# Optimization experiments

Measured on AMD Instinct MI355X. Metric: run time of the kernel, lower is better.

The kernel has to match this reference:

```python
import math
import jax, jax.numpy as jnp
import numpy as np

B, S, D, H, E = 4, 1024, 1024, 16, 8
HD = D // H


def gelu_new(x):
    # BERT/GPT tanh-approx GELU (NewGELUActivation)
    c = math.sqrt(2.0 / math.pi)
    return 0.5 * x * (1.0 + jnp.tanh(c * (x + 0.044715 * x ** 3)))


def setup_inputs() -> dict:
    key = jax.random.key(0)
    ks = jax.random.split(key, 12)
    s = 0.02
    return {
        "x": jax.random.normal(ks[0], (B, S, D), jnp.float32),
        "Wq": jax.random.normal(ks[1], (D, D), jnp.float32) * s,
        "bq": jnp.zeros((D,), jnp.float32),
        "Wk": jax.random.normal(ks[2], (D, D), jnp.float32) * s,
        "bk": jnp.zeros((D,), jnp.float32),
        "Wv": jax.random.normal(ks[3], (D, D), jnp.float32) * s,
        "bv": jnp.zeros((D,), jnp.float32),
        "Wg": jax.random.normal(ks[4], (D, E), jnp.float32) * s,
        "bg": jnp.zeros((E,), jnp.float32),
        "W1": jax.random.normal(ks[5], (E, D, D), jnp.float32) * s,
        "b1": jnp.zeros((E, D), jnp.float32),
        "W2": jax.random.normal(ks[6], (E, D, D), jnp.float32) * s,
        "b2": jnp.zeros((E, D), jnp.float32),
    }


def reference(x, Wq, bq, Wk, bk, Wv, bv, Wg, bg, W1, b1, W2, b2):
    b = x.shape[0]
    # ---- Attention (faithful to original: no head transpose, so attention
    # is computed ACROSS HEADS per token: scores are [B,S,H,H]) ----
    Q = (x @ Wq + bq).reshape(b, -1, H, HD)
    K = (x @ Wk + bk).reshape(b, -1, H, HD)
    V = (x @ Wv + bv).reshape(b, -1, H, HD)
    scores = jnp.einsum('bsqd,bskd->bsqk', Q, K) / (HD ** 0.5)  # [B,S,H,H]
    attn = jax.nn.softmax(scores, axis=-1)
    out = jnp.einsum('bsqk,bskd->bsqd', attn, V)  # [B,S,H,HD]
    # torch: out.transpose(1,2).contiguous().view(B,-1,H*HD)
    a = jnp.transpose(out, (0, 2, 1, 3)).reshape(b, -1, D)  # [B,S,D]

    # ---- ComplexMoE: dense all-experts + sequence-mean gating ----
    gates = jax.nn.softmax(a.mean(axis=1) @ Wg + bg, axis=-1)  # [B,E]
    h = gelu_new(jnp.einsum('bsd,edh->bseh', a, W1) + b1)       # [B,S,E,D]
    eo = jnp.einsum('bseh,ehf->bsef', h, W2) + b2               # [B,S,E,D]
    return jnp.einsum('be,bsed->bsd', gates, eo)                # [B,S,D]
```

## Files before the change

kernel.cpp:

```cpp
#include <hip/hip_runtime.h>
#include <stdint.h>

#define AS1 __attribute__((address_space(1)))
#define AS3 __attribute__((address_space(3)))

typedef short v8s __attribute__((ext_vector_type(8)));
typedef float v4f __attribute__((ext_vector_type(4)));

__device__ __forceinline__ float b2f(unsigned short u) {
  return __uint_as_float(((unsigned int)u) << 16);
}
__device__ __forceinline__ unsigned short f2bu(float f) {
  unsigned int u = __float_as_uint(f);
  u += 0x7fffu + ((u >> 16) & 1u);
  return (unsigned short)(u >> 16);
}

__device__ __forceinline__ void gload16(const void* g, const void* l) {
  __builtin_amdgcn_global_load_lds(
      (const AS1 void*)(uintptr_t)g,
      (AS3 void*)(unsigned)(uintptr_t)l,
      16, 0, 0);
}

#define BAR __builtin_amdgcn_s_barrier()
#define VMC2 asm volatile("s_waitcnt vmcnt(2)" ::: "memory")
#define VMC0 asm volatile("s_waitcnt vmcnt(0)" ::: "memory")

__global__ __launch_bounds__(256)
void transpose_cvt(const float* __restrict__ src, long long srcZ,
                   unsigned short* __restrict__ dst, long long dstZ, int ld_dst,
                   int K, int N)
{
  __shared__ float t[64][65];
  const int e = blockIdx.z;
  src += (long long)e * srcZ;
  dst += (long long)e * dstZ;
  const int k0 = blockIdx.y * 64, n0 = blockIdx.x * 64;
  const int tr  = threadIdx.x >> 4;
  const int tc4 = (threadIdx.x & 15) * 4;
#pragma unroll
  for (int p = 0; p < 4; ++p) {
    float4 v = *(const float4*)(src + (long long)(k0 + tr + p * 16) * N + n0 + tc4);
    t[tr + p * 16][tc4 + 0] = v.x;
    t[tr + p * 16][tc4 + 1] = v.y;
    t[tr + p * 16][tc4 + 2] = v.z;
    t[tr + p * 16][tc4 + 3] = v.w;
  }
  __syncthreads();
#pragma unroll
  for (int p = 0; p < 4; ++p) {
    const int n = tr + p * 16;
    ushort4 o;
    o.x = f2bu(t[tc4 + 0][n]);
    o.y = f2bu(t[tc4 + 1][n]);
    o.z = f2bu(t[tc4 + 2][n]);
    o.w = f2bu(t[tc4 + 3][n]);
    *(ushort4*)(dst + (long long)(n0 + n) * ld_dst + k0 + tc4) = o;
  }
}

__global__ __launch_bounds__(256)
void cvt_f32_bf16(const float* __restrict__ src, unsigned short* __restrict__ dst, int n)
{
  const int i = (blockIdx.x * 256 + threadIdx.x) * 4;
  if (i >= n) return;
  float4 v = *(const float4*)(src + i);
  ushort4 o;
  o.x = f2bu(v.x); o.y = f2bu(v.y); o.z = f2bu(v.z); o.w = f2bu(v.w);
  *(ushort4*)(dst + i) = o;
}

template<int MH>
__device__ __forceinline__ void read_a(v8s af[4][2],
    const unsigned short* pa, int wm, int rswz)
{
#pragma unroll
  for (int i = 0; i < 4; ++i)
#pragma unroll
    for (int s = 0; s < 2; ++s)
      af[i][s] = *(const v8s*)(pa + MH*8192 + ((((wm*4 + i)*2 + s) << 9) | rswz));
}

template<int NH>
__device__ __forceinline__ void read_b(v8s bfr[2][2],
    const unsigned short* pb, int wn, int rswz)
{
#pragma unroll
  for (int j = 0; j < 2; ++j)
#pragma unroll
    for (int s = 0; s < 2; ++s)
      bfr[j][s] = *(const v8s*)(pb + NH*8192 + ((((wn*2 + j)*2 + s) << 9) | rswz));
}

template<int MH, int NH>
__device__ __forceinline__ void mfma16(v4f acc[8][4], v8s af[4][2], v8s bfr[2][2])
{
  __builtin_amdgcn_s_setprio(1);
#pragma unroll
  for (int i = 0; i < 4; ++i)
#pragma unroll
    for (int j = 0; j < 2; ++j)
#pragma unroll
      for (int s = 0; s < 2; ++s)
        acc[MH*4+i][NH*2+j] = __builtin_amdgcn_mfma_f32_16x16x32_bf16(
            af[i][s], bfr[j][s], acc[MH*4+i][NH*2+j], 0, 0, 0);
  __builtin_amdgcn_s_setprio(0);
}

#define STAGE(G, LD, LDSBASE, GROW0, KT) do { \
    gload16((G) + (long long)((GROW0) + sRow) * (LD) + (KT) + sCol, \
            (LDSBASE) + w512); \
    gload16((G) + (long long)((GROW0) + 64 + sRow) * (LD) + (KT) + sCol, \
            (LDSBASE) + 4096 + w512); \
  } while (0)

template<int EPI>
__global__ __launch_bounds__(512, 2)
void gemm256(const unsigned short* __restrict__ A, int lda,
             const unsigned short* __restrict__ Bt, int ldb,
             const float* __restrict__ bias,
             void* __restrict__ out0, unsigned short* __restrict__ pbs,
             int kLen, const float* __restrict__ gates)
{
  __shared__ __align__(16) unsigned short lds[65536];
  unsigned short* As0 = lds;
  unsigned short* As1 = lds + 16384;
  unsigned short* Bs0 = lds + 32768;
  unsigned short* Bs1 = lds + 49152;

  const int tid  = threadIdx.x;
  const int lane = tid & 63;
  const int w    = tid >> 6;
  const int wm   = w >> 2;
  const int wn   = w & 3;
  const int m0   = blockIdx.y * 256;
  const int n0   = blockIdx.x * 256;
  const int z    = blockIdx.z;
  const int kBase = (EPI == 3) ? z * kLen : 0;

  const int sRow = (w >> 1) * 16 + (lane >> 2);
  const int sCol = (w & 1) * 32 + (((lane & 3) * 8) ^ (((lane >> 5) & 1) << 4));
  const int rr   = lane & 15;
  const int kgrp = lane >> 4;
  const int rswz = (rr * 32 + kgrp * 8) ^ ((rr & 8) << 1);
  const int w512 = w * 512;

  v4f acc[8][4] = {};
  v8s af[4][2], b0[2][2], b1[2][2];

  const int iters = kLen >> 7;

  STAGE(A,  lda, As0,        m0,       kBase);
  STAGE(A,  lda, As0 + 8192, m0 + 128, kBase);
  STAGE(Bt, ldb, Bs0,        n0,       kBase);
  STAGE(Bt, ldb, Bs0 + 8192, n0 + 128, kBase);
  STAGE(A,  lda, As1,        m0,       kBase + 64);
  VMC2;
  BAR;

  for (int it = 0; it < iters; ++it) {
    const bool nl = (it != iters - 1);
    const int k0t = kBase + it * 128;
    const int kT1 = k0t + 64, kT2 = k0t + 128, kT3 = k0t + 192;

    read_a<0>(af, As0, wm, rswz);
    read_b<0>(b0, Bs0, wn, rswz);
    STAGE(Bt, ldb, Bs1, n0, kT1);
    mfma16<0,0>(acc, af, b0);
    BAR;
    read_b<1>(b1, Bs0, wn, rswz);
    STAGE(Bt, ldb, Bs1 + 8192, n0 + 128, kT1);
    mfma16<0,1>(acc, af, b1);
    BAR;
    read_a<1>(af, As0, wm, rswz);
    STAGE(A, lda, As1 + 8192, m0 + 128, kT1);
    mfma16<1,1>(acc, af, b1);
    BAR;
    if (nl) STAGE(A, lda, As0, m0, kT2);
    mfma16<1,0>(acc, af, b0);
    if (nl) { VMC2; } else { VMC0; }
    BAR;
    read_a<0>(af, As1, wm, rswz);
    read_b<0>(b0, Bs1, wn, rswz);
    if (nl) STAGE(Bt, ldb, Bs0, n0, kT2);
    mfma16<0,0>(acc, af, b0);
    BAR;
    read_b<1>(b1, Bs1, wn, rswz);
    if (nl) STAGE(Bt, ldb, Bs0 + 8192, n0 + 128, kT2);
    mfma16<0,1>(acc, af, b1);
    BAR;
    read_a<1>(af, As1, wm, rswz);
    if (nl) STAGE(A, lda, As0 + 8192, m0 + 128, kT2);
    mfma16<1,1>(acc, af, b1);
    BAR;
    if (nl) STAGE(A, lda, As1, m0, kT3);
    mfma16<1,0>(acc, af, b0);
    if (nl) { VMC2; }
    BAR;
  }

  const int lr4 = (lane >> 4) * 4;
  const int lc  = lane & 15;
  float gate = 0.f;
  if (EPI == 1) gate = gates[(m0 >> 10) * 8 + (n0 >> 10)];

#pragma unroll
  for (int mi = 0; mi < 8; ++mi) {
    const int rowb = m0 + (mi >> 2) * 128 + wm * 64 + (mi & 3) * 16 + lr4;
#pragma unroll
    for (int nj = 0; nj < 4; ++nj) {
      const int col = n0 + (nj >> 1) * 128 + wn * 32 + (nj & 1) * 16 + lc;
#pragma unroll
      for (int r = 0; r < 4; ++r) {
        const int row = rowb + r;
        float v = acc[mi][nj][r];
        if (EPI == 0) {
          v += bias[col];
          const int which = col >> 10;
          ((unsigned short*)out0)[(long long)which * 4194304 + (long long)row * 1024 + (col & 1023)] = f2bu(v);
        } else if (EPI == 1) {
          v += bias[col];
          float u = 0.7978845608028654f * (v + 0.044715f * v * v * v);
          u = fminf(fmaxf(u, -15.f), 15.f);
          float e2 = __expf(2.f * u);
          float th = (e2 - 1.f) / (e2 + 1.f);
          ((unsigned short*)out0)[(long long)row * 8192 + col] = f2bu(gate * 0.5f * v * (1.f + th));
        } else {
          if (z == 0) ((float*)out0)[(long long)row * 1024 + col] = v;
          else pbs[(long long)(z - 1) * 4194304 + (long long)row * 1024 + col] = f2bu(v);
        }
      }
    }
  }
}

__global__ __launch_bounds__(256)
void reduce3(float* __restrict__ out, const unsigned short* __restrict__ pb,
             const float* __restrict__ bias2)
{
  const int i = (blockIdx.x * 256 + threadIdx.x) * 4;
  const int b = i >> 20;
  const int n = i & 1023;
  float4 a = *(const float4*)(out + i);
  ushort4 p0 = *(const ushort4*)(pb + i);
  ushort4 p1 = *(const ushort4*)(pb + 4194304 + i);
  ushort4 p2 = *(const ushort4*)(pb + 8388608 + i);
  float4 bb = *(const float4*)(bias2 + b * 1024 + n);
  a.x += b2f(p0.x) + b2f(p1.x) + b2f(p2.x) + bb.x;
  a.y += b2f(p0.y) + b2f(p1.y) + b2f(p2.y) + bb.y;
  a.z += b2f(p0.z) + b2f(p1.z) + b2f(p2.z) + bb.z;
  a.w += b2f(p0.w) + b2f(p1.w) + b2f(p2.w) + bb.w;
  *(float4*)(out + i) = a;
}

__global__ __launch_bounds__(256)
void attn_kernel(const unsigned short* __restrict__ Qb,
                 const unsigned short* __restrict__ Kb,
                 const unsigned short* __restrict__ Vb,
                 unsigned short* __restrict__ a)
{
  const int token = blockIdx.x;
  const int b = token >> 10, s = token & 1023;
  __shared__ float Qs[16][65], Ks[16][65], Vs[16][65];
  __shared__ float attn_s[16][17];
  const int t = threadIdx.x;
  const long long base = (long long)token * 1024;

  {
    const int i0 = t * 4;
    const int hh = i0 >> 6, dd = i0 & 63;
    ushort4 qv = *(const ushort4*)(Qb + base + i0);
    ushort4 kv = *(const ushort4*)(Kb + base + i0);
    ushort4 vv = *(const ushort4*)(Vb + base + i0);
    Qs[hh][dd+0]=b2f(qv.x); Qs[hh][dd+1]=b2f(qv.y); Qs[hh][dd+2]=b2f(qv.z); Qs[hh][dd+3]=b2f(qv.w);
    Ks[hh][dd+0]=b2f(kv.x); Ks[hh][dd+1]=b2f(kv.y); Ks[hh][dd+2]=b2f(kv.z); Ks[hh][dd+3]=b2f(kv.w);
    Vs[hh][dd+0]=b2f(vv.x); Vs[hh][dd+1]=b2f(vv.y); Vs[hh][dd+2]=b2f(vv.z); Vs[hh][dd+3]=b2f(vv.w);
  }
  __syncthreads();

  const int q = t >> 4, k = t & 15;
  float sc = 0.f;
#pragma unroll
  for (int d = 0; d < 64; ++d) sc += Qs[q][d] * Ks[k][d];
  sc *= 0.125f;
  float mx = sc;
#pragma unroll
  for (int m = 1; m < 16; m <<= 1) mx = fmaxf(mx, __shfl_xor(mx, m, 64));
  float ex = __expf(sc - mx);
  float sum = ex;
#pragma unroll
  for (int m = 1; m < 16; m <<= 1) sum += __shfl_xor(sum, m, 64);
  attn_s[q][k] = ex / sum;
  __syncthreads();

  const int hd = t & 63;
  const int wv = t >> 6;
#pragma unroll
  for (int r = 0; r < 4; ++r) {
    const int qq = wv * 4 + r;
    float o = 0.f;
#pragma unroll
    for (int kk = 0; kk < 16; ++kk) o += attn_s[qq][kk] * Vs[kk][hd];
    a[(long long)b * 1048576 + (long long)(qq * 64 + (s >> 4)) * 1024 + (s & 15) * 64 + hd] = f2bu(o);
  }
}

__global__ __launch_bounds__(256)
void col_sum_part(const unsigned short* __restrict__ a, float* __restrict__ part)
{
  const int bx = blockIdx.x;
  const int b = bx >> 2;
  const int d = (bx & 3) * 256 + threadIdx.x;
  const int y = blockIdx.y;
  const unsigned short* p = a + (long long)b * 1048576 + (long long)y * 131072 + d;
  float s = 0.f;
  for (int i = 0; i < 128; ++i) s += b2f(p[i * 1024]);
  part[(y * 4 + b) * 1024 + d] = s;
}

__global__ __launch_bounds__(256)
void gates_bias2(const float* __restrict__ part,
                 const float* __restrict__ Wg,
                 const float* __restrict__ bg,
                 const float* __restrict__ b2,
                 float* __restrict__ gates,
                 float* __restrict__ bias2)
{
  __shared__ float am[4][1024];
  __shared__ float sg[4][8];
  const int t = threadIdx.x;

  for (int i = t; i < 4096; i += 256) {
    const int b = i >> 10, d = i & 1023;
    float s = 0.f;
#pragma unroll
    for (int y = 0; y < 8; ++y) s += part[(y * 4 + b) * 1024 + d];
    am[b][d] = s * (1.f / 1024.f);
  }
  __syncthreads();

  const int pair = t >> 3, subl = t & 7;
  const int b = pair >> 3, e = pair & 7;
  float s = 0.f;
  for (int d = subl * 128; d < subl * 128 + 128; ++d) s += am[b][d] * Wg[d * 8 + e];
#pragma unroll
  for (int m = 1; m < 8; m <<= 1) s += __shfl_xor(s, m, 64);
  if (subl == 0) sg[b][e] = s + bg[e];
  __syncthreads();

  if (t < 4) {
    float mx = -1e30f;
    for (int ee = 0; ee < 8; ++ee) mx = fmaxf(mx, sg[t][ee]);
    float g[8]; float ssum = 0.f;
    for (int ee = 0; ee < 8; ++ee) { g[ee] = __expf(sg[t][ee] - mx); ssum += g[ee]; }
    for (int ee = 0; ee < 8; ++ee) { sg[t][ee] = g[ee] / ssum; gates[t * 8 + ee] = sg[t][ee]; }
  }
  __syncthreads();

  for (int i = t; i < 4096; i += 256) {
    const int bb = i >> 10, n = i & 1023;
    float ss = 0.f;
#pragma unroll
    for (int ee = 0; ee < 8; ++ee) ss += sg[bb][ee] * b2[ee * 1024 + n];
    bias2[i] = ss;
  }
}

extern "C" void kernel_launch(void* const* d_in, const int* in_sizes, int n_in,
                              void* d_out, int out_size, void* d_ws, size_t ws_size,
                              hipStream_t stream) {
  const float* x  = (const float*)d_in[0];
  const float* Wq = (const float*)d_in[1];
  const float* bq = (const float*)d_in[2];
  const float* Wk = (const float*)d_in[3];
  const float* bk = (const float*)d_in[4];
  const float* Wv = (const float*)d_in[5];
  const float* bv = (const float*)d_in[6];
  const float* Wg = (const float*)d_in[7];
  const float* bg = (const float*)d_in[8];
  const float* W1 = (const float*)d_in[9];
  const float* b1 = (const float*)d_in[10];
  const float* W2 = (const float*)d_in[11];
  const float* b2 = (const float*)d_in[12];
  float* out = (float*)d_out;

  if (ws_size < (size_t)109300000) return;

  char* ws = (char*)d_ws;
  unsigned short* xb   = (unsigned short*)(ws + 0);
  unsigned short* Wqt  = (unsigned short*)(ws + 8388608);
  unsigned short* Qb   = (unsigned short*)(ws + 14680064);
  unsigned short* hs   = (unsigned short*)(ws + 0);
  unsigned short* abuf = (unsigned short*)(ws + 67108864);
  unsigned short* pbs  = (unsigned short*)(ws + 67108864);
  unsigned short* W1t  = (unsigned short*)(ws + 75497472);
  unsigned short* W2t  = (unsigned short*)(ws + 92274688);
  float* part  = (float*)(ws + 109051904);
  float* gates = (float*)(ws + 109051904 + 131072);
  float* bias2 = (float*)(ws + 109051904 + 131072 + 512);
  float* bqkv  = (float*)(ws + 109051904 + 131072 + 512 + 16384);

  dim3 tb(256);

  transpose_cvt<<<dim3(16,16,1), tb, 0, stream>>>(Wq, 0LL, Wqt,           0LL, 1024, 1024, 1024);
  transpose_cvt<<<dim3(16,16,1), tb, 0, stream>>>(Wk, 0LL, Wqt + 1048576, 0LL, 1024, 1024, 1024);
  transpose_cvt<<<dim3(16,16,1), tb, 0, stream>>>(Wv, 0LL, Wqt + 2097152, 0LL, 1024, 1024, 1024);
  transpose_cvt<<<dim3(16,16,8), tb, 0, stream>>>(W1, 1048576LL, W1t, 1048576LL, 1024, 1024, 1024);
  transpose_cvt<<<dim3(16,16,8), tb, 0, stream>>>(W2, 1048576LL, W2t, 1024LL,    8192, 1024, 1024);
  cvt_f32_bf16<<<4096, tb, 0, stream>>>(x, xb, 4194304);
  hipMemcpyAsync(bqkv,        bq, 4096, hipMemcpyDeviceToDevice, stream);
  hipMemcpyAsync(bqkv + 1024, bk, 4096, hipMemcpyDeviceToDevice, stream);
  hipMemcpyAsync(bqkv + 2048, bv, 4096, hipMemcpyDeviceToDevice, stream);

  gemm256<0><<<dim3(12,16,1), 512, 0, stream>>>(xb, 1024, Wqt, 1024, bqkv,
                                                Qb, nullptr, 1024, nullptr);
  attn_kernel<<<4096, tb, 0, stream>>>(Qb, Qb + 4194304, Qb + 8388608, abuf);
  col_sum_part<<<dim3(16,8), tb, 0, stream>>>(abuf, part);
  gates_bias2<<<1, tb, 0, stream>>>(part, Wg, bg, b2, gates, bias2);
  gemm256<1><<<dim3(32,16,1), 512, 0, stream>>>(abuf, 1024, W1t, 1024, b1,
                                                hs, nullptr, 1024, gates);
  gemm256<3><<<dim3(4,16,4), 512, 0, stream>>>(hs, 8192, W2t, 8192, nullptr,
                                               out, pbs, 2048, nullptr);
  reduce3<<<4096, tb, 0, stream>>>(out, pbs, bias2);
}
```

Measured before the change: 263.9 us.

## Merge weight transposes into one launch, hoist B reads, vectorize column sum

```diff
diff --git a/kernel.cpp b/kernel.cpp
--- a/kernel.cpp
+++ b/kernel.cpp
@@ -28,20 +28,37 @@
 #define VMC0 asm volatile("s_waitcnt vmcnt(0)" ::: "memory")
 
 __global__ __launch_bounds__(256)
-void transpose_cvt(const float* __restrict__ src, long long srcZ,
-                   unsigned short* __restrict__ dst, long long dstZ, int ld_dst,
-                   int K, int N)
+void transpose_all(const float* __restrict__ wq, const float* __restrict__ wk,
+                   const float* __restrict__ wv, const float* __restrict__ w1,
+                   const float* __restrict__ w2,
+                   unsigned short* __restrict__ Wqt,
+                   unsigned short* __restrict__ W1t,
+                   unsigned short* __restrict__ W2t)
 {
   __shared__ float t[64][65];
-  const int e = blockIdx.z;
-  src += (long long)e * srcZ;
-  dst += (long long)e * dstZ;
+  const int z = blockIdx.z;
+  const float* src;
+  unsigned short* dst;
+  int ld;
+  if (z < 3) {
+    src = (z == 0) ? wq : (z == 1) ? wk : wv;
+    dst = Wqt + (long long)z * 1048576;
+    ld = 1024;
+  } else if (z < 11) {
+    src = w1 + (long long)(z - 3) * 1048576;
+    dst = W1t + (long long)(z - 3) * 1048576;
+    ld = 1024;
+  } else {
+    src = w2 + (long long)(z - 11) * 1048576;
+    dst = W2t + (long long)(z - 11) * 1024;
+    ld = 8192;
+  }
   const int k0 = blockIdx.y * 64, n0 = blockIdx.x * 64;
   const int tr  = threadIdx.x >> 4;
   const int tc4 = (threadIdx.x & 15) * 4;
 #pragma unroll
   for (int p = 0; p < 4; ++p) {
-    float4 v = *(const float4*)(src + (long long)(k0 + tr + p * 16) * N + n0 + tc4);
+    float4 v = *(const float4*)(src + (long long)(k0 + tr + p * 16) * 1024 + n0 + tc4);
     t[tr + p * 16][tc4 + 0] = v.x;
     t[tr + p * 16][tc4 + 1] = v.y;
     t[tr + p * 16][tc4 + 2] = v.z;
@@ -56,7 +73,7 @@
     o.y = f2bu(t[tc4 + 1][n]);
     o.z = f2bu(t[tc4 + 2][n]);
     o.w = f2bu(t[tc4 + 3][n]);
-    *(ushort4*)(dst + (long long)(n0 + n) * ld_dst + k0 + tc4) = o;
+    *(ushort4*)(dst + (long long)(n0 + n) * ld + k0 + tc4) = o;
   }
 }
 
@@ -166,10 +183,10 @@
 
     read_a<0>(af, As0, wm, rswz);
     read_b<0>(b0, Bs0, wn, rswz);
+    read_b<1>(b1, Bs0, wn, rswz);
     STAGE(Bt, ldb, Bs1, n0, kT1);
     mfma16<0,0>(acc, af, b0);
     BAR;
-    read_b<1>(b1, Bs0, wn, rswz);
     STAGE(Bt, ldb, Bs1 + 8192, n0 + 128, kT1);
     mfma16<0,1>(acc, af, b1);
     BAR;
@@ -183,10 +200,10 @@
     BAR;
     read_a<0>(af, As1, wm, rswz);
     read_b<0>(b0, Bs1, wn, rswz);
+    read_b<1>(b1, Bs1, wn, rswz);
     if (nl) STAGE(Bt, ldb, Bs0, n0, kT2);
     mfma16<0,0>(acc, af, b0);
     BAR;
-    read_b<1>(b1, Bs1, wn, rswz);
     if (nl) STAGE(Bt, ldb, Bs0 + 8192, n0 + 128, kT2);
     mfma16<0,1>(acc, af, b1);
     BAR;
@@ -309,14 +326,17 @@
 __global__ __launch_bounds__(256)
 void col_sum_part(const unsigned short* __restrict__ a, float* __restrict__ part)
 {
-  const int bx = blockIdx.x;
-  const int b = bx >> 2;
-  const int d = (bx & 3) * 256 + threadIdx.x;
+  const int b = blockIdx.x;
   const int y = blockIdx.y;
-  const unsigned short* p = a + (long long)b * 1048576 + (long long)y * 131072 + d;
-  float s = 0.f;
-  for (int i = 0; i < 128; ++i) s += b2f(p[i * 1024]);
-  part[(y * 4 + b) * 1024 + d] = s;
+  const int d4 = threadIdx.x * 4;
+  const unsigned short* p = a + (long long)b * 1048576 + (long long)y * 131072 + d4;
+  float s0 = 0.f, s1 = 0.f, s2 = 0.f, s3 = 0.f;
+  for (int i = 0; i < 128; ++i) {
+    ushort4 v = *(const ushort4*)(p + i * 1024);
+    s0 += b2f(v.x); s1 += b2f(v.y); s2 += b2f(v.z); s3 += b2f(v.w);
+  }
+  float* o = part + (y * 4 + b) * 1024 + d4;
+  o[0] = s0; o[1] = s1; o[2] = s2; o[3] = s3;
 }
 
 __global__ __launch_bounds__(256)
@@ -403,11 +423,7 @@
 
   dim3 tb(256);
 
-  transpose_cvt<<<dim3(16,16,1), tb, 0, stream>>>(Wq, 0LL, Wqt,           0LL, 1024, 1024, 1024);
-  transpose_cvt<<<dim3(16,16,1), tb, 0, stream>>>(Wk, 0LL, Wqt + 1048576, 0LL, 1024, 1024, 1024);
-  transpose_cvt<<<dim3(16,16,1), tb, 0, stream>>>(Wv, 0LL, Wqt + 2097152, 0LL, 1024, 1024, 1024);
-  transpose_cvt<<<dim3(16,16,8), tb, 0, stream>>>(W1, 1048576LL, W1t, 1048576LL, 1024, 1024, 1024);
-  transpose_cvt<<<dim3(16,16,8), tb, 0, stream>>>(W2, 1048576LL, W2t, 1024LL,    8192, 1024, 1024);
+  transpose_all<<<dim3(16,16,19), tb, 0, stream>>>(Wq, Wk, Wv, W1, W2, Wqt, W1t, W2t);
   cvt_f32_bf16<<<4096, tb, 0, stream>>>(x, xb, 4194304);
   hipMemcpyAsync(bqkv,        bq, 4096, hipMemcpyDeviceToDevice, stream);
   hipMemcpyAsync(bqkv + 1024, bk, 4096, hipMemcpyDeviceToDevice, stream);
@@ -416,7 +432,7 @@
   gemm256<0><<<dim3(12,16,1), 512, 0, stream>>>(xb, 1024, Wqt, 1024, bqkv,
                                                 Qb, nullptr, 1024, nullptr);
   attn_kernel<<<4096, tb, 0, stream>>>(Qb, Qb + 4194304, Qb + 8388608, abuf);
-  col_sum_part<<<dim3(16,8), tb, 0, stream>>>(abuf, part);
+  col_sum_part<<<dim3(4,8), tb, 0, stream>>>(abuf, part);
   gates_bias2<<<1, tb, 0, stream>>>(part, Wg, bg, b2, gates, bias2);
   gemm256<1><<<dim3(32,16,1), 512, 0, stream>>>(abuf, 1024, W1t, 1024, b1,
                                                 hs, nullptr, 1024, gates);
```

Measured after the change: 264.1 us, median of 2. Within noise of the previous version (+0.0%).
